# Kernel tuning notes

Hardware: AMD Instinct MI355X
Metric: run time of the kernel (lower is better)

Reference implementation:

```python
import jax, jax.numpy as jnp
import numpy as np

EMBED_DIM = 1024
PROJ_DIM = 256


def setup_inputs() -> dict:
    key = jax.random.key(0)
    kx, kq, kk = jax.random.split(key, 3)
    x = jax.random.normal(kx, (8, 4096, EMBED_DIM), dtype=jnp.float32)
    scale = 1.0 / (PROJ_DIM ** 0.5)
    q_proj = jax.random.normal(kq, (EMBED_DIM, PROJ_DIM), dtype=jnp.float32) * scale
    k_proj = jax.random.normal(kk, (EMBED_DIM, PROJ_DIM), dtype=jnp.float32) * scale
    return {"x": x, "q_proj": q_proj, "k_proj": k_proj}


def reference(x, q_proj, k_proj):
    # exp feature maps (FAVOR-style)
    q_prime = jnp.exp(jnp.einsum('bld,de->ble', x, q_proj))  # [B, L, E]
    k_prime = jnp.exp(jnp.einsum('bld,de->ble', x, k_proj))  # [B, L, E]
    # associative KV summary: O(L*E*D)
    kv = jnp.einsum('ble,bld->bed', k_prime, x)               # [B, E, D]
    num = jnp.einsum('ble,bed->bld', q_prime, kv)             # [B, L, D]
    z = 1.0 / (jnp.sum(q_prime, axis=-1, keepdims=True) + 1e-8)
    return num * z
```

## Files before the change

kernel.cpp:

```cpp
#include <hip/hip_runtime.h>


#define EMBED 1024
#define PROJ  256
#define LSEQ  4096
#define BATCH 8

typedef short  bfrag __attribute__((ext_vector_type(8)));
typedef float  f4    __attribute__((ext_vector_type(4)));
typedef unsigned short u16x8 __attribute__((ext_vector_type(8)));
typedef unsigned short u16x4 __attribute__((ext_vector_type(4)));

static __device__ __forceinline__ unsigned short f2bf(float f) {
  unsigned int u = __builtin_bit_cast(unsigned int, f);
  u += 0x7fffu + ((u >> 16) & 1u);
  return (unsigned short)(u >> 16);
}
static __device__ __forceinline__ float bf2f(unsigned short h) {
  unsigned int u = ((unsigned int)h) << 16;
  return __builtin_bit_cast(float, u);
}

static __device__ __forceinline__ void gload_lds16(const void* g, void* l) {
  __builtin_amdgcn_global_load_lds(
      (__attribute__((address_space(1))) void*)(unsigned long long)(g),
      (__attribute__((address_space(3))) void*)(unsigned)(unsigned long long)(l),
      16, 0, 0);
}

static __device__ __forceinline__ void stage_tile(
    const unsigned short* __restrict__ src, int row0, int stride, int k0,
    unsigned short* lds, int wave, int lane) {
#pragma unroll
  for (int j = 0; j < 4; j++) {
    int slot = (wave * 4 + j) * 64 + lane;
    int r = slot >> 3, cp = slot & 7;
    int c = cp ^ (r & 7);
    gload_lds16(src + (size_t)(row0 + r) * stride + k0 + c * 8,
                lds + (wave * 4 + j) * 512);
  }
}

static __device__ __forceinline__ void stage_tile_blk(
    const unsigned short* __restrict__ src, int row0, int ntcols, int k0,
    unsigned short* lds, int wave, int lane) {
#pragma unroll
  for (int j = 0; j < 4; j++) {
    int slot = (wave * 4 + j) * 64 + lane;
    int r = slot >> 3, cp = slot & 7;
    int c = cp ^ (r & 7);
    const unsigned short* blob =
        src + ((((size_t)(row0 >> 6) + (r >> 6)) * ntcols + (k0 >> 6)) << 12);
    gload_lds16(blob + ((r & 63) << 6) + c * 8, lds + (wave * 4 + j) * 512);
  }
}

static __device__ __forceinline__ bfrag read_frag(const unsigned short* lds,
                                                  int row, int chunk) {
  return *(const bfrag*)(lds + ((row << 3) + (chunk ^ (row & 7))) * 8);
}

__global__ __launch_bounds__(256) void cvtx_kernel(
    const float* __restrict__ x, unsigned short* __restrict__ xb,
    unsigned short* __restrict__ xT) {
  __shared__ unsigned short T[64 * 64];
  const int tid = threadIdx.x;
  const int d0 = blockIdx.x * 64, l0 = blockIdx.y * 64, b = blockIdx.z;
  const int mt = (b * LSEQ + l0) >> 6, dt = d0 >> 6;
  unsigned short* xbB = xb + (((size_t)mt * 16 + dt) << 12);
  unsigned short* xTB = xT + ((((size_t)b * 16 + dt) * 64 + (l0 >> 6)) << 12);
#pragma unroll
  for (int it = 0; it < 4; it++) {
    int slot = it * 256 + tid;
    int r = slot >> 4, c4 = slot & 15;
    f4 v = *(const f4*)(x + (size_t)(b * LSEQ + l0 + r) * EMBED + d0 + c4 * 4);
    u16x4 hv = (u16x4){f2bf(v[0]), f2bf(v[1]), f2bf(v[2]), f2bf(v[3])};
    *(u16x4*)(xbB + r * 64 + c4 * 4) = hv;
    const int g = ((r >> 2) ^ c4) << 2;
#pragma unroll
    for (int j = 0; j < 4; j++)
      T[(c4 * 4 + j) * 64 + g + (r & 3)] = hv[j];
  }
  __syncthreads();
#pragma unroll
  for (int it = 0; it < 2; it++) {
    int slot = it * 256 + tid;
    int dd = slot >> 3, ch = slot & 7;
    int q = dd >> 2;
    u16x4 lo = *(const u16x4*)(T + dd * 64 + (((2 * ch) ^ q) << 2));
    u16x4 hi = *(const u16x4*)(T + dd * 64 + (((2 * ch + 1) ^ q) << 2));
    u16x8 o = (u16x8){lo[0], lo[1], lo[2], lo[3], hi[0], hi[1], hi[2], hi[3]};
    *(u16x8*)(xTB + dd * 64 + ch * 8) = o;
  }
}

__global__ __launch_bounds__(256) void cvtw_kernel(
    const float* __restrict__ qw, const float* __restrict__ kw,
    unsigned short* __restrict__ wt) {
  __shared__ unsigned short T[64][72];
  const int tid = threadIdx.x;
  const int n0 = blockIdx.x * 64, k0 = blockIdx.y * 64;
  const float* W = blockIdx.z ? kw : qw;
#pragma unroll
  for (int it = 0; it < 4; it++) {
    int slot = it * 256 + tid;
    int r = slot >> 4, c4 = slot & 15;
    f4 v = *(const f4*)(W + (size_t)(k0 + r) * PROJ + n0 + c4 * 4);
#pragma unroll
    for (int j = 0; j < 4; j++) T[c4 * 4 + j][r] = f2bf(v[j]);
  }
  __syncthreads();
#pragma unroll
  for (int it = 0; it < 2; it++) {
    int slot = it * 256 + tid;
    int n = slot >> 3, ch = slot & 7;
    *(u16x8*)(wt + ((size_t)(blockIdx.z * PROJ + n0 + n)) * EMBED + k0 + ch * 8) =
        *(const u16x8*)&T[n][ch * 8];
  }
}

__global__ __launch_bounds__(256) void proj_kernel(
    const unsigned short* __restrict__ xb, const unsigned short* __restrict__ wt,
    unsigned short* __restrict__ qp, unsigned short* __restrict__ kT) {
  __shared__ union {
    struct { unsigned short A[128 * 64]; unsigned short B[128 * 64]; } t;
    unsigned short T[128 * 136];
  } sm;
  const int tid = threadIdx.x, wave = tid >> 6, lane = tid & 63;
  const int quad = lane >> 4, l16 = lane & 15;
  const int wm = wave >> 1, wn = wave & 1;
  const int n0 = blockIdx.x * 128, m0 = blockIdx.y * 128;

  f4 acc[4][4];
#pragma unroll
  for (int i = 0; i < 4; i++)
#pragma unroll
    for (int j = 0; j < 4; j++) acc[i][j] = (f4){0.f, 0.f, 0.f, 0.f};

  for (int k0 = 0; k0 < EMBED; k0 += 64) {
    stage_tile_blk(xb, m0, 16, k0, sm.t.A, wave, lane);
    stage_tile(wt, n0, EMBED, k0, sm.t.B, wave, lane);
    __syncthreads();
#pragma unroll
    for (int ks = 0; ks < 2; ks++) {
      bfrag a[4], bfr[4];
#pragma unroll
      for (int mt = 0; mt < 4; mt++)
        a[mt] = read_frag(sm.t.A, wm * 64 + mt * 16 + l16, ks * 4 + quad);
#pragma unroll
      for (int nt = 0; nt < 4; nt++)
        bfr[nt] = read_frag(sm.t.B, wn * 64 + nt * 16 + l16, ks * 4 + quad);
#pragma unroll
      for (int mt = 0; mt < 4; mt++)
#pragma unroll
        for (int nt = 0; nt < 4; nt++)
          acc[mt][nt] = __builtin_amdgcn_mfma_f32_16x16x32_bf16(
              a[mt], bfr[nt], acc[mt][nt], 0, 0, 0);
    }
    __syncthreads();
  }

  if (n0 < PROJ) {
#pragma unroll
    for (int mt = 0; mt < 4; mt++)
#pragma unroll
      for (int nt = 0; nt < 4; nt++)
#pragma unroll
        for (int r = 0; r < 4; r++)
          sm.T[(wm * 64 + mt * 16 + quad * 4 + r) * 136 + wn * 64 + nt * 16 + l16] =
              f2bf(__expf(acc[mt][nt][r]));
    __syncthreads();
#pragma unroll
    for (int it = 0; it < 8; it++) {
      int slot = it * 256 + tid;
      int row = slot >> 4, ch = slot & 15;
      *(u16x8*)(qp + (size_t)(m0 + row) * PROJ + n0 + ch * 8) =
          *(const u16x8*)&sm.T[row * 136 + ch * 8];
    }
  } else {
#pragma unroll
    for (int mt = 0; mt < 4; mt++)
#pragma unroll
      for (int nt = 0; nt < 4; nt++) {
        u16x4 h;
#pragma unroll
        for (int r = 0; r < 4; r++) h[r] = f2bf(__expf(acc[mt][nt][r]));
        *(u16x4*)&sm.T[(wn * 64 + nt * 16 + l16) * 136 + wm * 64 + mt * 16 + quad * 4] = h;
      }
    __syncthreads();
    const int bb = m0 >> 12, l0w = m0 & 4095, ebase = n0 - PROJ;
#pragma unroll
    for (int it = 0; it < 8; it++) {
      int cid = it * 256 + tid;
      int blobi = cid >> 9, within = cid & 511;
      int er = within >> 3, ch = within & 7;
      int e = (blobi >> 1) * 64 + er, lc = (blobi & 1) * 8 + ch;
      unsigned short* blob =
          kT + ((((size_t)bb * 4 + ((ebase >> 6) + (blobi >> 1))) * 64 +
                 (l0w >> 6) + (blobi & 1)) << 12);
      *(u16x8*)(blob + (er << 6) + ch * 8) = *(const u16x8*)&sm.T[e * 136 + lc * 8];
    }
  }
}

__global__ __launch_bounds__(256) void zinv_kernel(
    const unsigned short* __restrict__ qp, float* __restrict__ zinv) {
  int m = blockIdx.x * 4 + (threadIdx.x >> 6);
  int lane = threadIdx.x & 63;
  u16x4 h = *(const u16x4*)(qp + (size_t)m * PROJ + lane * 4);
  float s = bf2f(h[0]) + bf2f(h[1]) + bf2f(h[2]) + bf2f(h[3]);
#pragma unroll
  for (int off = 32; off; off >>= 1) s += __shfl_xor(s, off);
  if (lane == 0) zinv[m] = 1.0f / (s + 1e-8f);
}

__global__ __launch_bounds__(256) void kv_kernel(
    const unsigned short* __restrict__ kT, const unsigned short* __restrict__ xT,
    float* __restrict__ kvp) {
  __shared__ struct { unsigned short A[128 * 64]; unsigned short B[128 * 64]; } sm;
  const int tid = threadIdx.x, wave = tid >> 6, lane = tid & 63;
  const int quad = lane >> 4, l16 = lane & 15;
  const int wm = wave >> 1, wn = wave & 1;
  const int d0 = blockIdx.x * 128, e0 = blockIdx.y * 128;
  const int b = blockIdx.z & 7, split = blockIdx.z >> 3;
  const unsigned short* As = kT + ((size_t)b * 4 * 64 << 12);
  const unsigned short* Bs = xT + ((size_t)b * 16 * 64 << 12);

  f4 acc[4][4];
#pragma unroll
  for (int i = 0; i < 4; i++)
#pragma unroll
    for (int j = 0; j < 4; j++) acc[i][j] = (f4){0.f, 0.f, 0.f, 0.f};

  const int kbase = split * 1024;
  for (int kk = 0; kk < 1024; kk += 64) {
    stage_tile_blk(As, e0, 64, kbase + kk, sm.A, wave, lane);
    stage_tile_blk(Bs, d0, 64, kbase + kk, sm.B, wave, lane);
    __syncthreads();
#pragma unroll
    for (int ks = 0; ks < 2; ks++) {
      bfrag a[4], bfr[4];
#pragma unroll
      for (int mt = 0; mt < 4; mt++)
        a[mt] = read_frag(sm.A, wm * 64 + mt * 16 + l16, ks * 4 + quad);
#pragma unroll
      for (int nt = 0; nt < 4; nt++)
        bfr[nt] = read_frag(sm.B, wn * 64 + nt * 16 + l16, ks * 4 + quad);
#pragma unroll
      for (int mt = 0; mt < 4; mt++)
#pragma unroll
        for (int nt = 0; nt < 4; nt++)
          acc[mt][nt] = __builtin_amdgcn_mfma_f32_16x16x32_bf16(
              a[mt], bfr[nt], acc[mt][nt], 0, 0, 0);
    }
    __syncthreads();
  }

#pragma unroll
  for (int mt = 0; mt < 4; mt++)
#pragma unroll
    for (int nt = 0; nt < 4; nt++)
#pragma unroll
      for (int r = 0; r < 4; r++) {
        int e = e0 + wm * 64 + mt * 16 + quad * 4 + r;
        int d = d0 + wn * 64 + nt * 16 + l16;
        kvp[((size_t)(split * 8 + b) * PROJ + e) * EMBED + d] = acc[mt][nt][r];
      }
}

__global__ __launch_bounds__(256) void kvreduce_kernel(
    const float* __restrict__ kvp, unsigned short* __restrict__ kvT) {
  __shared__ float T[64][68];
  const int tid = threadIdx.x;
  const int d0 = blockIdx.x * 64, e0 = blockIdx.y * 64, b = blockIdx.z;
#pragma unroll
  for (int it = 0; it < 4; it++) {
    int slot = it * 256 + tid;
    int e = slot >> 4, c4 = slot & 15;
    f4 s = (f4){0.f, 0.f, 0.f, 0.f};
#pragma unroll
    for (int sp = 0; sp < 4; sp++)
      s += *(const f4*)(kvp + ((size_t)(sp * 8 + b) * PROJ + e0 + e) * EMBED + d0 + c4 * 4);
#pragma unroll
    for (int j = 0; j < 4; j++) T[c4 * 4 + j][e] = s[j];
  }
  __syncthreads();
#pragma unroll
  for (int it = 0; it < 2; it++) {
    int slot = it * 256 + tid;
    int d = slot >> 3, ch = slot & 7;
    u16x8 h;
#pragma unroll
    for (int j = 0; j < 8; j++) h[j] = f2bf(T[d][ch * 8 + j]);
    *(u16x8*)(kvT + ((size_t)(b * EMBED + d0 + d)) * PROJ + e0 + ch * 8) = h;
  }
}

__global__ __launch_bounds__(256) void out_kernel(
    const unsigned short* __restrict__ qp, const unsigned short* __restrict__ kvT,
    const float* __restrict__ zinv, float* __restrict__ out) {
  __shared__ struct { unsigned short A[128 * 64]; unsigned short B[128 * 64]; } sm;
  __shared__ float zv[128];
  const int tid = threadIdx.x, wave = tid >> 6, lane = tid & 63;
  const int quad = lane >> 4, l16 = lane & 15;
  const int wm = wave >> 1, wn = wave & 1;
  const int d0 = blockIdx.x * 128, l0 = blockIdx.y * 128, b = blockIdx.z;
  const unsigned short* As = qp + (size_t)b * LSEQ * PROJ;
  const unsigned short* Bs = kvT + (size_t)b * EMBED * PROJ;

  if (tid < 128) zv[tid] = zinv[b * LSEQ + l0 + tid];

  f4 acc[4][4];
#pragma unroll
  for (int i = 0; i < 4; i++)
#pragma unroll
    for (int j = 0; j < 4; j++) acc[i][j] = (f4){0.f, 0.f, 0.f, 0.f};

  for (int k0 = 0; k0 < PROJ; k0 += 64) {
    stage_tile(As, l0, PROJ, k0, sm.A, wave, lane);
    stage_tile(Bs, d0, PROJ, k0, sm.B, wave, lane);
    __syncthreads();
#pragma unroll
    for (int ks = 0; ks < 2; ks++) {
      bfrag a[4], bfr[4];
#pragma unroll
      for (int mt = 0; mt < 4; mt++)
        a[mt] = read_frag(sm.A, wm * 64 + mt * 16 + l16, ks * 4 + quad);
#pragma unroll
      for (int nt = 0; nt < 4; nt++)
        bfr[nt] = read_frag(sm.B, wn * 64 + nt * 16 + l16, ks * 4 + quad);
#pragma unroll
      for (int mt = 0; mt < 4; mt++)
#pragma unroll
        for (int nt = 0; nt < 4; nt++)
          acc[mt][nt] = __builtin_amdgcn_mfma_f32_16x16x32_bf16(
              a[mt], bfr[nt], acc[mt][nt], 0, 0, 0);
    }
    __syncthreads();
  }

#pragma unroll
  for (int mt = 0; mt < 4; mt++)
#pragma unroll
    for (int nt = 0; nt < 4; nt++)
#pragma unroll
      for (int r = 0; r < 4; r++) {
        int row = wm * 64 + mt * 16 + quad * 4 + r;
        int d = d0 + wn * 64 + nt * 16 + l16;
        out[((size_t)(b * LSEQ + l0 + row)) * EMBED + d] = acc[mt][nt][r] * zv[row];
      }
}

extern "C" void kernel_launch(void* const* d_in, const int* in_sizes, int n_in,
                              void* d_out, int out_size, void* d_ws, size_t ws_size,
                              hipStream_t stream) {
  const float* x  = (const float*)d_in[0];
  const float* qw = (const float*)d_in[1];
  const float* kw = (const float*)d_in[2];
  float* out = (float*)d_out;

  char* ws = (char*)d_ws;
  unsigned short* xb   = (unsigned short*)(ws);
  unsigned short* xT   = (unsigned short*)(ws + 67108864);
  unsigned short* wt   = (unsigned short*)(ws + 134217728);
  unsigned short* qp   = (unsigned short*)(ws + 135266304);
  unsigned short* kT   = (unsigned short*)(ws + 152043520);
  unsigned short* kvT  = (unsigned short*)(ws + 168820736);
  float*          zinv = (float*)(ws + 173015040);
  float*          kvp  = (float*)(ws);

  cvtx_kernel<<<dim3(16, 64, 8), 256, 0, stream>>>(x, xb, xT);
  cvtw_kernel<<<dim3(4, 16, 2), 256, 0, stream>>>(qw, kw, wt);
  proj_kernel<<<dim3(4, 256), 256, 0, stream>>>(xb, wt, qp, kT);
  zinv_kernel<<<dim3(8192), 256, 0, stream>>>(qp, zinv);
  kv_kernel<<<dim3(8, 2, 32), 256, 0, stream>>>(kT, xT, kvp);
  kvreduce_kernel<<<dim3(16, 4, 8), 256, 0, stream>>>(kvp, kvT);
  out_kernel<<<dim3(8, 32, 8), 256, 0, stream>>>(qp, kvT, zinv, out);
}
```

Baseline: 386.4 us.

## Drop global transposed x copy; transpose x tiles in LDS inside kv kernel

The conversion kernel becomes a plain row-major fp32-to-bf16 cast and no longer writes a blocked copy plus a transposed copy of x. The kv kernel now loads row-major x tiles and transposes them in shared memory before the MFMA loop, and the projection kernel reads row-major x through stage_tile. This removes a 64 MB global write and its later reread, at the cost of extra LDS traffic and two more barriers per k-step in the kv kernel. The kvp buffer moves into the freed xT region so it no longer aliases xb.

```diff
diff --git a/kernel.cpp b/kernel.cpp
--- a/kernel.cpp
+++ b/kernel.cpp
@@ -60,37 +60,17 @@
   return *(const bfrag*)(lds + ((row << 3) + (chunk ^ (row & 7))) * 8);
 }
 
-__global__ __launch_bounds__(256) void cvtx_kernel(
-    const float* __restrict__ x, unsigned short* __restrict__ xb,
-    unsigned short* __restrict__ xT) {
-  __shared__ unsigned short T[64 * 64];
-  const int tid = threadIdx.x;
-  const int d0 = blockIdx.x * 64, l0 = blockIdx.y * 64, b = blockIdx.z;
-  const int mt = (b * LSEQ + l0) >> 6, dt = d0 >> 6;
-  unsigned short* xbB = xb + (((size_t)mt * 16 + dt) << 12);
-  unsigned short* xTB = xT + ((((size_t)b * 16 + dt) * 64 + (l0 >> 6)) << 12);
-#pragma unroll
-  for (int it = 0; it < 4; it++) {
-    int slot = it * 256 + tid;
-    int r = slot >> 4, c4 = slot & 15;
-    f4 v = *(const f4*)(x + (size_t)(b * LSEQ + l0 + r) * EMBED + d0 + c4 * 4);
-    u16x4 hv = (u16x4){f2bf(v[0]), f2bf(v[1]), f2bf(v[2]), f2bf(v[3])};
-    *(u16x4*)(xbB + r * 64 + c4 * 4) = hv;
-    const int g = ((r >> 2) ^ c4) << 2;
-#pragma unroll
-    for (int j = 0; j < 4; j++)
-      T[(c4 * 4 + j) * 64 + g + (r & 3)] = hv[j];
-  }
-  __syncthreads();
-#pragma unroll
-  for (int it = 0; it < 2; it++) {
-    int slot = it * 256 + tid;
-    int dd = slot >> 3, ch = slot & 7;
-    int q = dd >> 2;
-    u16x4 lo = *(const u16x4*)(T + dd * 64 + (((2 * ch) ^ q) << 2));
-    u16x4 hi = *(const u16x4*)(T + dd * 64 + (((2 * ch + 1) ^ q) << 2));
-    u16x8 o = (u16x8){lo[0], lo[1], lo[2], lo[3], hi[0], hi[1], hi[2], hi[3]};
-    *(u16x8*)(xTB + dd * 64 + ch * 8) = o;
+__global__ __launch_bounds__(256) void cvtb_kernel(
+    const float* __restrict__ x, unsigned short* __restrict__ xb) {
+  const size_t total = (size_t)BATCH * LSEQ * EMBED;
+  size_t i = ((size_t)blockIdx.x * 256 + threadIdx.x) * 8;
+  const size_t stride = (size_t)gridDim.x * 256 * 8;
+  for (; i < total; i += stride) {
+    f4 a = *(const f4*)(x + i);
+    f4 b = *(const f4*)(x + i + 4);
+    u16x8 h = (u16x8){f2bf(a[0]), f2bf(a[1]), f2bf(a[2]), f2bf(a[3]),
+                      f2bf(b[0]), f2bf(b[1]), f2bf(b[2]), f2bf(b[3])};
+    *(u16x8*)(xb + i) = h;
   }
 }
 
@@ -138,7 +118,7 @@
     for (int j = 0; j < 4; j++) acc[i][j] = (f4){0.f, 0.f, 0.f, 0.f};
 
   for (int k0 = 0; k0 < EMBED; k0 += 64) {
-    stage_tile_blk(xb, m0, 16, k0, sm.t.A, wave, lane);
+    stage_tile(xb, m0, EMBED, k0, sm.t.A, wave, lane);
     stage_tile(wt, n0, EMBED, k0, sm.t.B, wave, lane);
     __syncthreads();
 #pragma unroll
@@ -215,16 +195,20 @@
 }
 
 __global__ __launch_bounds__(256) void kv_kernel(
-    const unsigned short* __restrict__ kT, const unsigned short* __restrict__ xT,
+    const unsigned short* __restrict__ kT, const unsigned short* __restrict__ xb,
     float* __restrict__ kvp) {
-  __shared__ struct { unsigned short A[128 * 64]; unsigned short B[128 * 64]; } sm;
+  __shared__ struct {
+    unsigned short A[128 * 64];
+    unsigned short B[128 * 64];
+    unsigned short T[2][64 * 64];
+  } sm;
   const int tid = threadIdx.x, wave = tid >> 6, lane = tid & 63;
   const int quad = lane >> 4, l16 = lane & 15;
   const int wm = wave >> 1, wn = wave & 1;
   const int d0 = blockIdx.x * 128, e0 = blockIdx.y * 128;
   const int b = blockIdx.z & 7, split = blockIdx.z >> 3;
   const unsigned short* As = kT + ((size_t)b * 4 * 64 << 12);
-  const unsigned short* Bs = xT + ((size_t)b * 16 * 64 << 12);
+  const unsigned short* xrow = xb + (size_t)b * LSEQ * EMBED;
 
   f4 acc[4][4];
 #pragma unroll
@@ -235,7 +219,37 @@
   const int kbase = split * 1024;
   for (int kk = 0; kk < 1024; kk += 64) {
     stage_tile_blk(As, e0, 64, kbase + kk, sm.A, wave, lane);
-    stage_tile_blk(Bs, d0, 64, kbase + kk, sm.B, wave, lane);
+#pragma unroll
+    for (int j = 0; j < 4; j++) {
+      int c = (wave * 4 + j) * 64 + lane;
+      int r = c >> 4, c16 = c & 15;
+      gload_lds16(xrow + (size_t)(kbase + kk + r) * EMBED + d0 + c16 * 8,
+                  sm.B + (wave * 4 + j) * 512);
+    }
+    __syncthreads();
+#pragma unroll
+    for (int sub = 0; sub < 2; sub++)
+#pragma unroll
+      for (int it = 0; it < 4; it++) {
+        int slot = it * 256 + tid;
+        int r = slot >> 4, c4 = slot & 15;
+        u16x4 v = *(const u16x4*)(sm.B + r * 128 + sub * 64 + c4 * 4);
+        int g = ((r >> 2) ^ c4) << 2;
+#pragma unroll
+        for (int j2 = 0; j2 < 4; j2++)
+          sm.T[sub][(c4 * 4 + j2) * 64 + g + (r & 3)] = v[j2];
+      }
+    __syncthreads();
+#pragma unroll
+    for (int it = 0; it < 4; it++) {
+      int slot = it * 256 + tid;
+      int d = slot >> 3, ch = slot & 7;
+      int sub = d >> 6, dl = d & 63, q = dl >> 2;
+      u16x4 lo = *(const u16x4*)(sm.T[sub] + dl * 64 + (((2 * ch) ^ q) << 2));
+      u16x4 hi = *(const u16x4*)(sm.T[sub] + dl * 64 + (((2 * ch + 1) ^ q) << 2));
+      u16x8 o = (u16x8){lo[0], lo[1], lo[2], lo[3], hi[0], hi[1], hi[2], hi[3]};
+      *(u16x8*)(sm.B + d * 64 + (ch ^ (d & 7)) * 8) = o;
+    }
     __syncthreads();
 #pragma unroll
     for (int ks = 0; ks < 2; ks++) {
@@ -361,19 +375,18 @@
 
   char* ws = (char*)d_ws;
   unsigned short* xb   = (unsigned short*)(ws);
-  unsigned short* xT   = (unsigned short*)(ws + 67108864);
+  float*          kvp  = (float*)(ws + 67108864);
   unsigned short* wt   = (unsigned short*)(ws + 134217728);
   unsigned short* qp   = (unsigned short*)(ws + 135266304);
   unsigned short* kT   = (unsigned short*)(ws + 152043520);
   unsigned short* kvT  = (unsigned short*)(ws + 168820736);
   float*          zinv = (float*)(ws + 173015040);
-  float*          kvp  = (float*)(ws);
-
-  cvtx_kernel<<<dim3(16, 64, 8), 256, 0, stream>>>(x, xb, xT);
+
+  cvtb_kernel<<<dim3(2048), 256, 0, stream>>>(x, xb);
   cvtw_kernel<<<dim3(4, 16, 2), 256, 0, stream>>>(qw, kw, wt);
   proj_kernel<<<dim3(4, 256), 256, 0, stream>>>(xb, wt, qp, kT);
   zinv_kernel<<<dim3(8192), 256, 0, stream>>>(qp, zinv);
-  kv_kernel<<<dim3(8, 2, 32), 256, 0, stream>>>(kT, xT, kvp);
+  kv_kernel<<<dim3(8, 2, 32), 256, 0, stream>>>(kT, xb, kvp);
   kvreduce_kernel<<<dim3(16, 4, 8), 256, 0, stream>>>(kvp, kvT);
   out_kernel<<<dim3(8, 32, 8), 256, 0, stream>>>(qp, kvT, zinv, out);
 }
```

Result: faster. 367.8 us (-4.8%).
